# Kernel optimization log

Measured on AMD Instinct MI355X. Metric: run time of the kernel, lower is better.

Reference implementation:

```python
import jax, jax.numpy as jnp
import numpy as np

NEG_BIG = -9.0e15  # matches torch zero_vec constant


def setup_inputs() -> dict:
    key = jax.random.key(0)
    k1, k2, k3, k4, k5 = jax.random.split(key, 5)
    B, N, D_IN, D_HID, D_OUT = 4, 4096, 128, 64, 128
    h = jax.random.normal(k1, (B, N, D_IN), dtype=jnp.float32)
    adj = jax.random.randint(k2, (N, N), 0, 2, dtype=jnp.int32)
    Ws = jax.random.normal(k3, (D_IN, D_HID), dtype=jnp.float32) * (1.414 / np.sqrt(D_IN))
    Wt = jax.random.normal(k4, (D_IN, D_HID), dtype=jnp.float32) * (1.414 / np.sqrt(D_IN))
    Wc = jax.random.normal(k5, (D_IN, D_OUT), dtype=jnp.float32) * np.sqrt(2.0 / D_IN)
    return {"h": h, "adj": adj, "Ws": Ws, "Wt": Wt, "Wc": Wc}


def reference(h, adj, Ws, Wt, Wc):
    # h: [B,N,D_in], adj: [N,N] broadcast over batch
    Whs = jnp.matmul(h, Ws)                     # [B,N,H]
    Wht = jnp.matmul(h, Wt)                     # [B,N,H]
    e = jnp.einsum('bnh,bmh->bnm', Whs, Wht)    # [B,N,N] dense scores
    z = jnp.where(adj > 0, e, NEG_BIG)          # adjacency mask
    alpha = jax.nn.softmax(z, axis=-1)          # [B,N,N]
    Whc = jnp.matmul(h, Wc)                     # [B,N,D_out]
    h_prime = jnp.matmul(alpha, Whc)            # [B,N,D_out]
    return h_prime
```

## Files before the change

kernel.cpp:

```cpp
#include <hip/hip_runtime.h>
#include <hip/hip_bf16.h>

#define NTOK 4096
#define BATCH 4
#define DIN 128
#define DHID 64
#define DOUT 128
#define NWRD (NTOK / 32)
#define SPLIT 4
#define ITERS (NTOK / SPLIT / 64)
#define NEG_BIG -9.0e15f

typedef short short8 __attribute__((ext_vector_type(8)));
typedef float floatx4 __attribute__((ext_vector_type(4)));

static __device__ __forceinline__ unsigned short f2bf(float f) {
    unsigned int u = __builtin_bit_cast(unsigned int, f);
    u = (u + 0x7fffu + ((u >> 16) & 1u)) >> 16;
    return (unsigned short)u;
}
static __device__ __forceinline__ float bf2f(unsigned short s) {
    unsigned int u = ((unsigned int)s) << 16;
    return __builtin_bit_cast(float, u);
}
static __device__ __forceinline__ unsigned int pk2(float lo, float hi) {
    unsigned int r;
    asm("v_cvt_pk_bf16_f32 %0, %1, %2" : "=v"(r) : "v"(lo), "v"(hi));
    return r;
}

static __device__ __forceinline__ floatx4 mfma16(short8 a, short8 b, floatx4 c) {
    return __builtin_amdgcn_mfma_f32_16x16x32_bf16(a, b, c, 0, 0, 0);
}

__global__ __launch_bounds__(256) void pack_adj_kernel(const int* __restrict__ adj,
                                                       unsigned int* __restrict__ bits) {
    int w = blockIdx.x * 256 + threadIdx.x;
    const int4* p = reinterpret_cast<const int4*>(adj) + (size_t)w * 8;
    unsigned int m = 0;
#pragma unroll
    for (int i = 0; i < 8; ++i) {
        int4 v = p[i];
        m |= (v.x > 0 ? 1u : 0u) << (4 * i + 0);
        m |= (v.y > 0 ? 1u : 0u) << (4 * i + 1);
        m |= (v.z > 0 ? 1u : 0u) << (4 * i + 2);
        m |= (v.w > 0 ? 1u : 0u) << (4 * i + 3);
    }
    bits[w] = m;
}

__global__ __launch_bounds__(256) void conv_w_kernel(const float* __restrict__ Ws,
                                                     const float* __restrict__ Wt,
                                                     const float* __restrict__ Wc,
                                                     unsigned short* __restrict__ WT_hi,
                                                     unsigned short* __restrict__ WT_lo) {
    int idx = blockIdx.x * 256 + threadIdx.x;
    int k = idx >> 8, col = idx & 255;
    float w;
    if (col < 64) w = Ws[k * DHID + col];
    else if (col < 128) w = Wt[k * DHID + (col - 64)];
    else w = Wc[k * DOUT + (col - 128)];
    unsigned short hi = f2bf(w);
    WT_hi[col * DIN + k] = hi;
    if (col < 128) WT_lo[col * DIN + k] = f2bf(w - bf2f(hi));
}

__global__ __launch_bounds__(256) void prep_kernel(const float* __restrict__ h,
                                                   const unsigned short* __restrict__ WT_hi,
                                                   const unsigned short* __restrict__ WT_lo,
                                                   unsigned short* __restrict__ Whs_hi,
                                                   unsigned short* __restrict__ Whs_lo,
                                                   unsigned short* __restrict__ Wht_hi,
                                                   unsigned short* __restrict__ Wht_lo,
                                                   unsigned short* __restrict__ WhcT) {
    int tid = threadIdx.x;
    int b = blockIdx.y;
    int w = tid >> 6, lane = tid & 63, lg = lane >> 4, lc = lane & 15;
    int n0 = blockIdx.x * 16;
    const float* hrow = h + (size_t)(b * NTOK + n0 + lc) * DIN;

    short8 ah[4], al[4];
#pragma unroll
    for (int ks = 0; ks < 4; ++ks) {
        float4 f0 = *reinterpret_cast<const float4*>(hrow + ks * 32 + lg * 8);
        float4 f1 = *reinterpret_cast<const float4*>(hrow + ks * 32 + lg * 8 + 4);
        float x[8] = {f0.x, f0.y, f0.z, f0.w, f1.x, f1.y, f1.z, f1.w};
        short8 hh, ll;
#pragma unroll
        for (int j = 0; j < 8; ++j) {
            unsigned short hb = f2bf(x[j]);
            hh[j] = (short)hb;
            ll[j] = (short)f2bf(x[j] - bf2f(hb));
        }
        ah[ks] = hh;
        al[ks] = ll;
    }

#pragma unroll
    for (int ci = 0; ci < 4; ++ci) {
        int ct = w * 4 + ci;
        int col = ct * 16 + lc;
        const unsigned short* bbase = WT_hi + (size_t)col * DIN;
        const unsigned short* lbase = WT_lo + (size_t)col * DIN;
        floatx4 acc = {0.f, 0.f, 0.f, 0.f};
#pragma unroll
        for (int ks = 0; ks < 4; ++ks) {
            short8 bh = *reinterpret_cast<const short8*>(bbase + ks * 32 + lg * 8);
            acc = mfma16(ah[ks], bh, acc);
            if (w < 2) {
                short8 bl = *reinterpret_cast<const short8*>(lbase + ks * 32 + lg * 8);
                acc = mfma16(ah[ks], bl, acc);
                acc = mfma16(al[ks], bh, acc);
            }
        }
        int nr = n0 + 4 * lg;
        if (w == 0) {
#pragma unroll
            for (int r = 0; r < 4; ++r) {
                float v = acc[r];
                unsigned short hb = f2bf(v);
                size_t o = (size_t)(b * NTOK + nr + r) * DHID + col;
                Whs_hi[o] = hb;
                Whs_lo[o] = f2bf(v - bf2f(hb));
            }
        } else if (w == 1) {
#pragma unroll
            for (int r = 0; r < 4; ++r) {
                float v = acc[r];
                unsigned short hb = f2bf(v);
                size_t o = (size_t)(b * NTOK + nr + r) * DHID + (col - 64);
                Wht_hi[o] = hb;
                Wht_lo[o] = f2bf(v - bf2f(hb));
            }
        } else {
            unsigned int p01 = (unsigned int)f2bf(acc[0]) | ((unsigned int)f2bf(acc[1]) << 16);
            unsigned int p23 = (unsigned int)f2bf(acc[2]) | ((unsigned int)f2bf(acc[3]) << 16);
            unsigned int* dst =
                reinterpret_cast<unsigned int*>(&WhcT[(size_t)(b * DOUT + col - 128) * NTOK + nr]);
            dst[0] = p01;
            dst[1] = p23;
        }
    }
}

__global__ __launch_bounds__(256, 2) void attn_kernel(const unsigned short* __restrict__ Whs_hi,
                                                      const unsigned short* __restrict__ Whs_lo,
                                                      const unsigned short* __restrict__ Wht_hi,
                                                      const unsigned short* __restrict__ Wht_lo,
                                                      const unsigned short* __restrict__ WhcT,
                                                      const unsigned int* __restrict__ bits,
                                                      unsigned short* __restrict__ po,
                                                      float* __restrict__ pm,
                                                      float* __restrict__ pl) {
    __shared__ unsigned short Kh_lds[64][72];
    __shared__ unsigned short Kl_lds[64][72];
    __shared__ unsigned short V_lds[128][72];

    int tid = threadIdx.x;
    int b = blockIdx.y;
    int split = blockIdx.z;
    int kbase = split * (NTOK / SPLIT);
    int lane = tid & 63, lg = lane >> 4, lc = lane & 15;
    int q0 = blockIdx.x * 128 + (tid >> 6) * 32;
    int nA = q0 + lc, nB = q0 + 16 + lc;

    const unsigned short* qAH = Whs_hi + (size_t)(b * NTOK + nA) * DHID;
    const unsigned short* qAL = Whs_lo + (size_t)(b * NTOK + nA) * DHID;
    const unsigned short* qBH = Whs_hi + (size_t)(b * NTOK + nB) * DHID;
    const unsigned short* qBL = Whs_lo + (size_t)(b * NTOK + nB) * DHID;
    short8 qAh0 = *reinterpret_cast<const short8*>(qAH + lg * 8);
    short8 qAh1 = *reinterpret_cast<const short8*>(qAH + 32 + lg * 8);
    short8 qAl0 = *reinterpret_cast<const short8*>(qAL + lg * 8);
    short8 qAl1 = *reinterpret_cast<const short8*>(qAL + 32 + lg * 8);
    short8 qBh0 = *reinterpret_cast<const short8*>(qBH + lg * 8);
    short8 qBh1 = *reinterpret_cast<const short8*>(qBH + 32 + lg * 8);
    short8 qBl0 = *reinterpret_cast<const short8*>(qBL + lg * 8);
    short8 qBl1 = *reinterpret_cast<const short8*>(qBL + 32 + lg * 8);

    floatx4 o0[8], o1[8];
#pragma unroll
    for (int dt = 0; dt < 8; ++dt) {
        o0[dt] = (floatx4){0.f, 0.f, 0.f, 0.f};
        o1[dt] = (floatx4){0.f, 0.f, 0.f, 0.f};
    }
    float mA = NEG_BIG, lA = 0.f, mB = NEG_BIG, lB = 0.f;

    int kkey = tid >> 2, koff = (tid & 3) * 16;
    int vd = tid >> 1, va = tid & 1;

    short8 krH0, krH1, krL0, krL1, vr0, vr1, vr2, vr3;
    unsigned int mwA0, mwA1, mwB0, mwB1;

    {
        int kb = kbase;
        const unsigned short* ksrcH = Wht_hi + (size_t)(b * NTOK + kb + kkey) * DHID + koff;
        const unsigned short* ksrcL = Wht_lo + (size_t)(b * NTOK + kb + kkey) * DHID + koff;
        krH0 = *reinterpret_cast<const short8*>(ksrcH);
        krH1 = *reinterpret_cast<const short8*>(ksrcH + 8);
        krL0 = *reinterpret_cast<const short8*>(ksrcL);
        krL1 = *reinterpret_cast<const short8*>(ksrcL + 8);
        const unsigned short* vsrc = WhcT + (size_t)(b * DOUT + vd) * NTOK + kb + va * 32;
        vr0 = *reinterpret_cast<const short8*>(vsrc);
        vr1 = *reinterpret_cast<const short8*>(vsrc + 8);
        vr2 = *reinterpret_cast<const short8*>(vsrc + 16);
        vr3 = *reinterpret_cast<const short8*>(vsrc + 24);
        mwA0 = bits[nA * NWRD + (kb >> 5)];
        mwA1 = bits[nA * NWRD + (kb >> 5) + 1];
        mwB0 = bits[nB * NWRD + (kb >> 5)];
        mwB1 = bits[nB * NWRD + (kb >> 5) + 1];
    }

    for (int it = 0; it < ITERS; ++it) {
        __syncthreads();
        *reinterpret_cast<short8*>(&Kh_lds[kkey][koff]) = krH0;
        *reinterpret_cast<short8*>(&Kh_lds[kkey][koff + 8]) = krH1;
        *reinterpret_cast<short8*>(&Kl_lds[kkey][koff]) = krL0;
        *reinterpret_cast<short8*>(&Kl_lds[kkey][koff + 8]) = krL1;
        {
            int sb = va * 32;
            short8 w00 = __builtin_shufflevector(vr0, vr2, 0, 1, 2, 3, 8, 9, 10, 11);
            short8 w01 = __builtin_shufflevector(vr0, vr2, 4, 5, 6, 7, 12, 13, 14, 15);
            short8 w10 = __builtin_shufflevector(vr1, vr3, 0, 1, 2, 3, 8, 9, 10, 11);
            short8 w11 = __builtin_shufflevector(vr1, vr3, 4, 5, 6, 7, 12, 13, 14, 15);
            *reinterpret_cast<short8*>(&V_lds[vd][sb]) = w00;
            *reinterpret_cast<short8*>(&V_lds[vd][sb + 8]) = w01;
            *reinterpret_cast<short8*>(&V_lds[vd][sb + 16]) = w10;
            *reinterpret_cast<short8*>(&V_lds[vd][sb + 24]) = w11;
        }
        __syncthreads();

        floatx4 s0[4], s1[4];
        __builtin_amdgcn_s_setprio(1);
#pragma unroll
        for (int kc = 0; kc < 4; ++kc) {
            short8 kh0 = *reinterpret_cast<const short8*>(&Kh_lds[kc * 16 + lc][lg * 8]);
            short8 kh1 = *reinterpret_cast<const short8*>(&Kh_lds[kc * 16 + lc][32 + lg * 8]);
            short8 kl0 = *reinterpret_cast<const short8*>(&Kl_lds[kc * 16 + lc][lg * 8]);
            short8 kl1 = *reinterpret_cast<const short8*>(&Kl_lds[kc * 16 + lc][32 + lg * 8]);
            floatx4 a0 = {0.f, 0.f, 0.f, 0.f};
            a0 = mfma16(kh0, qAh0, a0);
            a0 = mfma16(kh1, qAh1, a0);
            a0 = mfma16(kh0, qAl0, a0);
            a0 = mfma16(kh1, qAl1, a0);
            a0 = mfma16(kl0, qAh0, a0);
            a0 = mfma16(kl1, qAh1, a0);
            s0[kc] = a0;
            floatx4 a1 = {0.f, 0.f, 0.f, 0.f};
            a1 = mfma16(kh0, qBh0, a1);
            a1 = mfma16(kh1, qBh1, a1);
            a1 = mfma16(kh0, qBl0, a1);
            a1 = mfma16(kh1, qBl1, a1);
            a1 = mfma16(kl0, qBh0, a1);
            a1 = mfma16(kl1, qBh1, a1);
            s1[kc] = a1;
        }
        __builtin_amdgcn_s_setprio(0);

#pragma unroll
        for (int kc = 0; kc < 4; ++kc) {
            unsigned int wA = (kc & 2) ? mwA1 : mwA0;
            unsigned int wB = (kc & 2) ? mwB1 : mwB0;
#pragma unroll
            for (int r = 0; r < 4; ++r) {
                int bit = 16 * (kc & 1) + 4 * lg + r;
                if (!((wA >> bit) & 1u)) s0[kc][r] = NEG_BIG;
                if (!((wB >> bit) & 1u)) s1[kc][r] = NEG_BIG;
            }
        }

        if (it + 1 < ITERS) {
            int kb = kbase + (it + 1) * 64;
            const unsigned short* ksrcH = Wht_hi + (size_t)(b * NTOK + kb + kkey) * DHID + koff;
            const unsigned short* ksrcL = Wht_lo + (size_t)(b * NTOK + kb + kkey) * DHID + koff;
            krH0 = *reinterpret_cast<const short8*>(ksrcH);
            krH1 = *reinterpret_cast<const short8*>(ksrcH + 8);
            krL0 = *reinterpret_cast<const short8*>(ksrcL);
            krL1 = *reinterpret_cast<const short8*>(ksrcL + 8);
            const unsigned short* vsrc = WhcT + (size_t)(b * DOUT + vd) * NTOK + kb + va * 32;
            vr0 = *reinterpret_cast<const short8*>(vsrc);
            vr1 = *reinterpret_cast<const short8*>(vsrc + 8);
            vr2 = *reinterpret_cast<const short8*>(vsrc + 16);
            vr3 = *reinterpret_cast<const short8*>(vsrc + 24);
            mwA0 = bits[nA * NWRD + (kb >> 5)];
            mwA1 = bits[nA * NWRD + (kb >> 5) + 1];
            mwB0 = bits[nB * NWRD + (kb >> 5)];
            mwB1 = bits[nB * NWRD + (kb >> 5) + 1];
        }

        float scA, scB;
        {
            float vm = s0[0][0];
#pragma unroll
            for (int kc = 0; kc < 4; ++kc)
#pragma unroll
                for (int r = 0; r < 4; ++r) vm = fmaxf(vm, s0[kc][r]);
            vm = fmaxf(vm, __shfl_xor(vm, 16));
            vm = fmaxf(vm, __shfl_xor(vm, 32));
            float mn = fmaxf(mA, vm);
            scA = __expf(mA - mn);
            mA = mn;
            float rs = 0.f;
#pragma unroll
            for (int kc = 0; kc < 4; ++kc)
#pragma unroll
                for (int r = 0; r < 4; ++r) {
                    float p = __expf(s0[kc][r] - mn);
                    s0[kc][r] = p;
                    rs += p;
                }
            rs += __shfl_xor(rs, 16);
            rs += __shfl_xor(rs, 32);
            lA = lA * scA + rs;
        }
        {
            float vm = s1[0][0];
#pragma unroll
            for (int kc = 0; kc < 4; ++kc)
#pragma unroll
                for (int r = 0; r < 4; ++r) vm = fmaxf(vm, s1[kc][r]);
            vm = fmaxf(vm, __shfl_xor(vm, 16));
            vm = fmaxf(vm, __shfl_xor(vm, 32));
            float mn = fmaxf(mB, vm);
            scB = __expf(mB - mn);
            mB = mn;
            float rs = 0.f;
#pragma unroll
            for (int kc = 0; kc < 4; ++kc)
#pragma unroll
                for (int r = 0; r < 4; ++r) {
                    float p = __expf(s1[kc][r] - mn);
                    s1[kc][r] = p;
                    rs += p;
                }
            rs += __shfl_xor(rs, 16);
            rs += __shfl_xor(rs, 32);
            lB = lB * scB + rs;
        }

        {
            float sc4[4];
#pragma unroll
            for (int r = 0; r < 4; ++r) sc4[r] = __shfl(scA, (lane & 48) + 4 * lg + r);
#pragma unroll
            for (int dt = 0; dt < 8; ++dt)
#pragma unroll
                for (int r = 0; r < 4; ++r) o0[dt][r] *= sc4[r];
#pragma unroll
            for (int r = 0; r < 4; ++r) sc4[r] = __shfl(scB, (lane & 48) + 4 * lg + r);
#pragma unroll
            for (int dt = 0; dt < 8; ++dt)
#pragma unroll
                for (int r = 0; r < 4; ++r) o1[dt][r] *= sc4[r];
        }

        unsigned int pw[8];
        pw[0] = pk2(s0[0][0], s0[0][1]); pw[1] = pk2(s0[0][2], s0[0][3]);
        pw[2] = pk2(s0[1][0], s0[1][1]); pw[3] = pk2(s0[1][2], s0[1][3]);
        pw[4] = pk2(s0[2][0], s0[2][1]); pw[5] = pk2(s0[2][2], s0[2][3]);
        pw[6] = pk2(s0[3][0], s0[3][1]); pw[7] = pk2(s0[3][2], s0[3][3]);
        short8 paA0 = __builtin_bit_cast(short8, *reinterpret_cast<uint4*>(&pw[0]));
        short8 paA1 = __builtin_bit_cast(short8, *reinterpret_cast<uint4*>(&pw[4]));
        pw[0] = pk2(s1[0][0], s1[0][1]); pw[1] = pk2(s1[0][2], s1[0][3]);
        pw[2] = pk2(s1[1][0], s1[1][1]); pw[3] = pk2(s1[1][2], s1[1][3]);
        pw[4] = pk2(s1[2][0], s1[2][1]); pw[5] = pk2(s1[2][2], s1[2][3]);
        pw[6] = pk2(s1[3][0], s1[3][1]); pw[7] = pk2(s1[3][2], s1[3][3]);
        short8 paB0 = __builtin_bit_cast(short8, *reinterpret_cast<uint4*>(&pw[0]));
        short8 paB1 = __builtin_bit_cast(short8, *reinterpret_cast<uint4*>(&pw[4]));

        __builtin_amdgcn_s_setprio(1);
#pragma unroll
        for (int dt = 0; dt < 8; ++dt) {
            short8 vf0 = *reinterpret_cast<const short8*>(&V_lds[dt * 16 + lc][lg * 8]);
            o0[dt] = mfma16(paA0, vf0, o0[dt]);
            o1[dt] = mfma16(paB0, vf0, o1[dt]);
        }
#pragma unroll
        for (int dt = 0; dt < 8; ++dt) {
            short8 vf1 = *reinterpret_cast<const short8*>(&V_lds[dt * 16 + lc][32 + lg * 8]);
            o0[dt] = mfma16(paA1, vf1, o0[dt]);
            o1[dt] = mfma16(paB1, vf1, o1[dt]);
        }
        __builtin_amdgcn_s_setprio(0);
    }

    {
        float m4[4], l4[4];
#pragma unroll
        for (int r = 0; r < 4; ++r) {
            int src = (lane & 48) + 4 * lg + r;
            m4[r] = __shfl(mA, src);
            l4[r] = __shfl(lA, src);
        }
#pragma unroll
        for (int r = 0; r < 4; ++r) {
            size_t row = (size_t)(split * BATCH + b) * NTOK + q0 + 4 * lg + r;
            unsigned short* prow = po + row * DOUT;
#pragma unroll
            for (int dt = 0; dt < 8; ++dt) prow[dt * 16 + lc] = f2bf(o0[dt][r]);
            if (lc == 0) {
                pm[row] = m4[r];
                pl[row] = l4[r];
            }
        }
#pragma unroll
        for (int r = 0; r < 4; ++r) {
            int src = (lane & 48) + 4 * lg + r;
            m4[r] = __shfl(mB, src);
            l4[r] = __shfl(lB, src);
        }
#pragma unroll
        for (int r = 0; r < 4; ++r) {
            size_t row = (size_t)(split * BATCH + b) * NTOK + q0 + 16 + 4 * lg + r;
            unsigned short* prow = po + row * DOUT;
#pragma unroll
            for (int dt = 0; dt < 8; ++dt) prow[dt * 16 + lc] = f2bf(o1[dt][r]);
            if (lc == 0) {
                pm[row] = m4[r];
                pl[row] = l4[r];
            }
        }
    }
}

__global__ __launch_bounds__(256) void merge_kernel(const unsigned short* __restrict__ po,
                                                    const float* __restrict__ pm,
                                                    const float* __restrict__ pl,
                                                    float* __restrict__ out) {
    int idx = blockIdx.x * 256 + threadIdx.x;
    int d = idx & (DOUT - 1);
    size_t bn = (size_t)(idx >> 7);
    const size_t BN = (size_t)BATCH * NTOK;

    float ms[SPLIT];
#pragma unroll
    for (int s = 0; s < SPLIT; ++s) ms[s] = pm[s * BN + bn];
    float M = ms[0];
#pragma unroll
    for (int s = 1; s < SPLIT; ++s) M = fmaxf(M, ms[s]);
    float L = 0.f, acc = 0.f;
#pragma unroll
    for (int s = 0; s < SPLIT; ++s) {
        float e = __expf(ms[s] - M);
        L += pl[s * BN + bn] * e;
        acc += bf2f(po[(s * BN + bn) * DOUT + d]) * e;
    }
    out[idx] = acc / L;
}

extern "C" void kernel_launch(void* const* d_in, const int* in_sizes, int n_in,
                              void* d_out, int out_size, void* d_ws, size_t ws_size,
                              hipStream_t stream) {
    const float* h   = (const float*)d_in[0];
    const int*   adj = (const int*)d_in[1];
    const float* Ws  = (const float*)d_in[2];
    const float* Wt  = (const float*)d_in[3];
    const float* Wc  = (const float*)d_in[4];
    float* out = (float*)d_out;

    size_t nq = (size_t)BATCH * NTOK * DHID;
    unsigned short* Whs_hi = (unsigned short*)d_ws;
    unsigned short* Whs_lo = Whs_hi + nq;
    unsigned short* Wht_hi = Whs_lo + nq;
    unsigned short* Wht_lo = Wht_hi + nq;
    unsigned short* WhcT   = Wht_lo + nq;
    unsigned int*   bits   = (unsigned int*)(WhcT + (size_t)BATCH * DOUT * NTOK);
    unsigned short* WT_hi  = (unsigned short*)(bits + (size_t)NTOK * NWRD);
    unsigned short* WT_lo  = WT_hi + 256 * DIN;
    unsigned short* po     = WT_lo + 128 * DIN;
    float*          pm     = (float*)(po + (size_t)SPLIT * BATCH * NTOK * DOUT);
    float*          pl     = pm + (size_t)SPLIT * BATCH * NTOK;

    pack_adj_kernel<<<dim3(NTOK * NWRD / 256), dim3(256), 0, stream>>>(adj, bits);
    conv_w_kernel<<<dim3(128), dim3(256), 0, stream>>>(Ws, Wt, Wc, WT_hi, WT_lo);
    prep_kernel<<<dim3(NTOK / 16, BATCH), dim3(256), 0, stream>>>(
        h, WT_hi, WT_lo, Whs_hi, Whs_lo, Wht_hi, Wht_lo, WhcT);
    attn_kernel<<<dim3(NTOK / 128, BATCH, SPLIT), dim3(256), 0, stream>>>(
        Whs_hi, Whs_lo, Wht_hi, Wht_lo, WhcT, bits, po, pm, pl);
    merge_kernel<<<dim3(BATCH * NTOK * DOUT / 256), dim3(256), 0, stream>>>(po, pm, pl, out);
}
```

Measured before the change: 189.5 us.

## Use exp2 with prescaled queries, lazy rescaling, and workspace-dependent split-K

Result: slower. 200.0 us (+5.6%).

```diff
diff --git a/kernel.cpp b/kernel.cpp
--- a/kernel.cpp
+++ b/kernel.cpp
@@ -7,9 +7,8 @@
 #define DHID 64
 #define DOUT 128
 #define NWRD (NTOK / 32)
-#define SPLIT 4
-#define ITERS (NTOK / SPLIT / 64)
 #define NEG_BIG -9.0e15f
+#define LOG2E 1.44269504088896340736f
 
 typedef short short8 __attribute__((ext_vector_type(8)));
 typedef float floatx4 __attribute__((ext_vector_type(4)));
@@ -57,7 +56,7 @@
     int idx = blockIdx.x * 256 + threadIdx.x;
     int k = idx >> 8, col = idx & 255;
     float w;
-    if (col < 64) w = Ws[k * DHID + col];
+    if (col < 64) w = Ws[k * DHID + col] * LOG2E;
     else if (col < 128) w = Wt[k * DHID + (col - 64)];
     else w = Wc[k * DOUT + (col - 128)];
     unsigned short hi = f2bf(w);
@@ -143,6 +142,7 @@
     }
 }
 
+template <int ITERS>
 __global__ __launch_bounds__(256, 2) void attn_kernel(const unsigned short* __restrict__ Whs_hi,
                                                       const unsigned short* __restrict__ Whs_lo,
                                                       const unsigned short* __restrict__ Wht_hi,
@@ -159,7 +159,7 @@
     int tid = threadIdx.x;
     int b = blockIdx.y;
     int split = blockIdx.z;
-    int kbase = split * (NTOK / SPLIT);
+    int kbase = split * (ITERS * 64);
     int lane = tid & 63, lg = lane >> 4, lc = lane & 15;
     int q0 = blockIdx.x * 128 + (tid >> 6) * 32;
     int nA = q0 + lc, nB = q0 + 16 + lc;
@@ -287,7 +287,6 @@
             mwB1 = bits[nB * NWRD + (kb >> 5) + 1];
         }
 
-        float scA, scB;
         {
             float vm = s0[0][0];
 #pragma unroll
@@ -296,21 +295,33 @@
                 for (int r = 0; r < 4; ++r) vm = fmaxf(vm, s0[kc][r]);
             vm = fmaxf(vm, __shfl_xor(vm, 16));
             vm = fmaxf(vm, __shfl_xor(vm, 32));
-            float mn = fmaxf(mA, vm);
-            scA = __expf(mA - mn);
-            mA = mn;
+            bool skip = __all(vm <= mA + 4.0f);
+            float mn = skip ? mA : fmaxf(mA, vm);
             float rs = 0.f;
 #pragma unroll
             for (int kc = 0; kc < 4; ++kc)
 #pragma unroll
                 for (int r = 0; r < 4; ++r) {
-                    float p = __expf(s0[kc][r] - mn);
+                    float p = exp2f(s0[kc][r] - mn);
                     s0[kc][r] = p;
                     rs += p;
                 }
             rs += __shfl_xor(rs, 16);
             rs += __shfl_xor(rs, 32);
-            lA = lA * scA + rs;
+            if (!skip) {
+                float sc = exp2f(mA - mn);
+                lA = lA * sc + rs;
+                mA = mn;
+                float sc4[4];
+#pragma unroll
+                for (int r = 0; r < 4; ++r) sc4[r] = __shfl(sc, (lane & 48) + 4 * lg + r);
+#pragma unroll
+                for (int dt = 0; dt < 8; ++dt)
+#pragma unroll
+                    for (int r = 0; r < 4; ++r) o0[dt][r] *= sc4[r];
+            } else {
+                lA += rs;
+            }
         }
         {
             float vm = s1[0][0];
@@ -320,37 +331,33 @@
                 for (int r = 0; r < 4; ++r) vm = fmaxf(vm, s1[kc][r]);
             vm = fmaxf(vm, __shfl_xor(vm, 16));
             vm = fmaxf(vm, __shfl_xor(vm, 32));
-            float mn = fmaxf(mB, vm);
-            scB = __expf(mB - mn);
-            mB = mn;
+            bool skip = __all(vm <= mB + 4.0f);
+            float mn = skip ? mB : fmaxf(mB, vm);
             float rs = 0.f;
 #pragma unroll
             for (int kc = 0; kc < 4; ++kc)
 #pragma unroll
                 for (int r = 0; r < 4; ++r) {
-                    float p = __expf(s1[kc][r] - mn);
+                    float p = exp2f(s1[kc][r] - mn);
                     s1[kc][r] = p;
                     rs += p;
                 }
             rs += __shfl_xor(rs, 16);
             rs += __shfl_xor(rs, 32);
-            lB = lB * scB + rs;
-        }
-
-        {
-            float sc4[4];
-#pragma unroll
-            for (int r = 0; r < 4; ++r) sc4[r] = __shfl(scA, (lane & 48) + 4 * lg + r);
-#pragma unroll
-            for (int dt = 0; dt < 8; ++dt)
-#pragma unroll
-                for (int r = 0; r < 4; ++r) o0[dt][r] *= sc4[r];
-#pragma unroll
-            for (int r = 0; r < 4; ++r) sc4[r] = __shfl(scB, (lane & 48) + 4 * lg + r);
-#pragma unroll
-            for (int dt = 0; dt < 8; ++dt)
-#pragma unroll
-                for (int r = 0; r < 4; ++r) o1[dt][r] *= sc4[r];
+            if (!skip) {
+                float sc = exp2f(mB - mn);
+                lB = lB * sc + rs;
+                mB = mn;
+                float sc4[4];
+#pragma unroll
+                for (int r = 0; r < 4; ++r) sc4[r] = __shfl(sc, (lane & 48) + 4 * lg + r);
+#pragma unroll
+                for (int dt = 0; dt < 8; ++dt)
+#pragma unroll
+                    for (int r = 0; r < 4; ++r) o1[dt][r] *= sc4[r];
+            } else {
+                lB += rs;
+            }
         }
 
         unsigned int pw[8];
@@ -422,6 +429,7 @@
     }
 }
 
+template <int NSPLIT>
 __global__ __launch_bounds__(256) void merge_kernel(const unsigned short* __restrict__ po,
                                                     const float* __restrict__ pm,
                                                     const float* __restrict__ pl,
@@ -431,16 +439,16 @@
     size_t bn = (size_t)(idx >> 7);
     const size_t BN = (size_t)BATCH * NTOK;
 
-    float ms[SPLIT];
-#pragma unroll
-    for (int s = 0; s < SPLIT; ++s) ms[s] = pm[s * BN + bn];
+    float ms[NSPLIT];
+#pragma unroll
+    for (int s = 0; s < NSPLIT; ++s) ms[s] = pm[s * BN + bn];
     float M = ms[0];
 #pragma unroll
-    for (int s = 1; s < SPLIT; ++s) M = fmaxf(M, ms[s]);
+    for (int s = 1; s < NSPLIT; ++s) M = fmaxf(M, ms[s]);
     float L = 0.f, acc = 0.f;
 #pragma unroll
-    for (int s = 0; s < SPLIT; ++s) {
-        float e = __expf(ms[s] - M);
+    for (int s = 0; s < NSPLIT; ++s) {
+        float e = exp2f(ms[s] - M);
         L += pl[s * BN + bn] * e;
         acc += bf2f(po[(s * BN + bn) * DOUT + d]) * e;
     }
@@ -467,14 +475,26 @@
     unsigned short* WT_hi  = (unsigned short*)(bits + (size_t)NTOK * NWRD);
     unsigned short* WT_lo  = WT_hi + 256 * DIN;
     unsigned short* po     = WT_lo + 128 * DIN;
-    float*          pm     = (float*)(po + (size_t)SPLIT * BATCH * NTOK * DOUT);
-    float*          pl     = pm + (size_t)SPLIT * BATCH * NTOK;
+    const size_t BASE = (size_t)((char*)po - (char*)d_ws);
+
+    size_t need8 = BASE + 8 * ((size_t)BATCH * NTOK * DOUT * 2 + (size_t)BATCH * NTOK * 8);
+    int use8 = (ws_size >= need8) ? 1 : 0;
+    int nsplit = use8 ? 8 : 4;
+
+    float* pm = (float*)(po + (size_t)nsplit * BATCH * NTOK * DOUT);
+    float* pl = pm + (size_t)nsplit * BATCH * NTOK;
 
     pack_adj_kernel<<<dim3(NTOK * NWRD / 256), dim3(256), 0, stream>>>(adj, bits);
     conv_w_kernel<<<dim3(128), dim3(256), 0, stream>>>(Ws, Wt, Wc, WT_hi, WT_lo);
     prep_kernel<<<dim3(NTOK / 16, BATCH), dim3(256), 0, stream>>>(
         h, WT_hi, WT_lo, Whs_hi, Whs_lo, Wht_hi, Wht_lo, WhcT);
-    attn_kernel<<<dim3(NTOK / 128, BATCH, SPLIT), dim3(256), 0, stream>>>(
-        Whs_hi, Whs_lo, Wht_hi, Wht_lo, WhcT, bits, po, pm, pl);
-    merge_kernel<<<dim3(BATCH * NTOK * DOUT / 256), dim3(256), 0, stream>>>(po, pm, pl, out);
-}
+    if (use8) {
+        attn_kernel<8><<<dim3(NTOK / 128, BATCH, 8), dim3(256), 0, stream>>>(
+            Whs_hi, Whs_lo, Wht_hi, Wht_lo, WhcT, bits, po, pm, pl);
+        merge_kernel<8><<<dim3(BATCH * NTOK * DOUT / 256), dim3(256), 0, stream>>>(po, pm, pl, out);
+    } else {
+        attn_kernel<16><<<dim3(NTOK / 128, BATCH, 4), dim3(256), 0, stream>>>(
+            Whs_hi, Whs_lo, Wht_hi, Wht_lo, WhcT, bits, po, pm, pl);
+        merge_kernel<4><<<dim3(BATCH * NTOK * DOUT / 256), dim3(256), 0, stream>>>(po, pm, pl, out);
+    }
+}
```
